# Performance work log

Measured on AMD Instinct MI355X. Metric: run time of the kernel, lower is better.

The kernel has to match this reference:

```python
import jax, jax.numpy as jnp
import numpy as np

LUT_DIM = 33
CTX_DIM = 128


def _identity_lut(dim):
    coords = jnp.linspace(0.0, 1.0, dim)
    r, g, b = jnp.meshgrid(coords, coords, coords, indexing='ij')
    return jnp.stack([r, g, b], axis=-1)  # [dim, dim, dim, 3], axes (r,g,b)


def setup_inputs() -> dict:
    key = jax.random.key(0)
    ks = jax.random.split(key, 8)
    B, H, W = 4, 512, 512
    image = jax.random.normal(ks[0], (B, 3, H, W), dtype=jnp.float32)
    spatial_context = jax.random.normal(ks[1], (B, CTX_DIM, H, W), dtype=jnp.float32)
    s = 0.05
    params = {
        'base_lut': _identity_lut(LUT_DIM),
        'W1': jax.random.normal(ks[2], (128, CTX_DIM), dtype=jnp.float32) * s,
        'b1': jnp.zeros((128,), dtype=jnp.float32),
        'W2': jax.random.normal(ks[3], (64, 128), dtype=jnp.float32) * s,
        'b2': jnp.zeros((64,), dtype=jnp.float32),
        'W3': jax.random.normal(ks[4], (3, 64), dtype=jnp.float32) * s,
        'b3': jnp.zeros((3,), dtype=jnp.float32),
        'offset_scale': jnp.float32(0.1),
    }
    return {'image': image, 'spatial_context': spatial_context, **params}


def _conv1x1(x, W, b):
    # x: [B,Cin,H,W], W: [Cout,Cin]
    return jnp.einsum('bchw,oc->bohw', x, W) + b[None, :, None, None]


def _trilinear_lut(lut_flat, gx, gy, gz, dim):
    # lut_flat: [3, dim^3] (flattened over z,y,x = r,g,b axes)
    # gx,gy,gz: [B,H,W] float coords in [0, dim-1]; border padding via clamp
    fmax = jnp.float32(dim - 1)
    gx = jnp.clip(gx, 0.0, fmax)
    gy = jnp.clip(gy, 0.0, fmax)
    gz = jnp.clip(gz, 0.0, fmax)
    x0 = jnp.floor(gx).astype(jnp.int32)
    y0 = jnp.floor(gy).astype(jnp.int32)
    z0 = jnp.floor(gz).astype(jnp.int32)
    x1 = jnp.minimum(x0 + 1, dim - 1)
    y1 = jnp.minimum(y0 + 1, dim - 1)
    z1 = jnp.minimum(z0 + 1, dim - 1)
    fx = gx - x0.astype(gx.dtype)
    fy = gy - y0.astype(gy.dtype)
    fz = gz - z0.astype(gz.dtype)

    def gather(zi, yi, xi):
        idx = (zi * dim + yi) * dim + xi  # [B,H,W]
        return lut_flat[:, idx]  # [3,B,H,W]

    c000 = gather(z0, y0, x0); c001 = gather(z0, y0, x1)
    c010 = gather(z0, y1, x0); c011 = gather(z0, y1, x1)
    c100 = gather(z1, y0, x0); c101 = gather(z1, y0, x1)
    c110 = gather(z1, y1, x0); c111 = gather(z1, y1, x1)

    fx = fx[None]; fy = fy[None]; fz = fz[None]
    c00 = c000 * (1 - fx) + c001 * fx
    c01 = c010 * (1 - fx) + c011 * fx
    c10 = c100 * (1 - fx) + c101 * fx
    c11 = c110 * (1 - fx) + c111 * fx
    c0 = c00 * (1 - fy) + c01 * fy
    c1 = c10 * (1 - fy) + c11 * fy
    out = c0 * (1 - fz) + c1 * fz  # [3,B,H,W]
    return jnp.transpose(out, (1, 0, 2, 3))  # [B,3,H,W]


def reference(image, spatial_context, base_lut, W1, b1, W2, b2, W3, b3, offset_scale):
    dim = base_lut.shape[0]
    gelu = lambda v: jax.nn.gelu(v, approximate=False)
    h = gelu(_conv1x1(spatial_context, W1, b1))
    h = gelu(_conv1x1(h, W2, b2))
    offset = jnp.tanh(_conv1x1(h, W3, b3)) * offset_scale  # [B,3,H,W]

    img01 = jnp.clip((image + 1.0) * 0.5, 0.0, 1.0)
    # grid_sample convention: grid channel0 (R)->x->last LUT axis (b),
    # channel1 (G)->y->g axis, channel2 (B)->z->r axis; align_corners=True.
    scale = jnp.float32(dim - 1)
    gx = img01[:, 0] * scale  # R -> b axis
    gy = img01[:, 1] * scale  # G -> g axis
    gz = img01[:, 2] * scale  # B -> r axis
    # base_lut [r,g,b,3] -> channels-first [3, r(=z), g(=y), b(=x)] -> flatten
    lut_flat = jnp.transpose(base_lut, (3, 0, 1, 2)).reshape(3, dim * dim * dim)
    sampled = _trilinear_lut(lut_flat, gx, gy, gz, dim)  # [B,3,H,W]
    return sampled * 2.0 - 1.0 + offset
```

## Files before the change

kernel.cpp:

```cpp
#include <hip/hip_runtime.h>
#include <stdint.h>

#define HW 262144
#define LDIM 33

typedef __bf16 bf16x8 __attribute__((ext_vector_type(8)));
typedef float  f32x4  __attribute__((ext_vector_type(4)));

union BF8 { bf16x8 v; unsigned u[4]; };

__device__ __forceinline__ unsigned bfr1(float a) {
  unsigned u = __float_as_uint(a);
  return (u + 0x7fffu + ((u >> 16) & 1u)) >> 16;
}
__device__ __forceinline__ unsigned pk2(float a, float b) {
  return bfr1(a) | (bfr1(b) << 16);
}
__device__ __forceinline__ float tanh_fast(float x) {
  return 1.0f - 2.0f / (__expf(2.0f * x) + 1.0f);
}
__device__ __forceinline__ float gelu_t(float x) {
  float t = tanh_fast(0.7978845608028654f * (x + 0.044715f * x * x * x));
  return 0.5f * x * (1.0f + t);
}

__global__ __launch_bounds__(256, 2) void local3dlut_kernel(
    const float* __restrict__ img,  const float* __restrict__ ctx,
    const float* __restrict__ lut,  const float* __restrict__ W1,
    const float* __restrict__ b1,   const float* __restrict__ W2,
    const float* __restrict__ b2,   const float* __restrict__ W3,
    const float* __restrict__ b3,   const float* __restrict__ oscp,
    float* __restrict__ out)
{
  __shared__ uint4 smem4[4096];
  char* sm = (char*)smem4;
  const int t    = threadIdx.x;
  const int lane = t & 63;
  const int wv   = t >> 6;
  const int n    = lane & 15;
  const int q    = lane >> 4;

  #pragma unroll
  for (int rep = 0; rep < 16; ++rep) {
    int f4 = t + 256 * rep;
    float4 v = ((const float4*)W1)[f4];
    int fi = f4 << 2;
    int o = fi >> 7, k = fi & 127;
    char* dst = sm + o * 256 + (((k >> 3) ^ (o & 15)) << 4) + ((k & 7) << 1);
    *(uint2*)dst = make_uint2(pk2(v.x, v.y), pk2(v.z, v.w));
  }
  #pragma unroll
  for (int rep = 0; rep < 8; ++rep) {
    int f4 = t + 256 * rep;
    float4 v = ((const float4*)W2)[f4];
    int fi = f4 << 2;
    int o = fi >> 7, k = fi & 127;
    char* dst = sm + 32768 + o * 256 + (((k >> 3) ^ (o & 15)) << 4) + ((k & 7) << 1);
    *(uint2*)dst = make_uint2(pk2(v.x, v.y), pk2(v.z, v.w));
  }
  __syncthreads();

  float b1r[8], b2r[4], w3r[3][4];
  #pragma unroll
  for (int i = 0; i < 8; ++i) b1r[i] = b1[i * 16 + n];
  #pragma unroll
  for (int i = 0; i < 4; ++i) b2r[i] = b2[i * 16 + n];
  #pragma unroll
  for (int j = 0; j < 3; ++j)
    #pragma unroll
    for (int i = 0; i < 4; ++i) w3r[j][i] = W3[j * 64 + i * 16 + n];
  const float b3r0 = b3[0], b3r1 = b3[1], b3r2 = b3[2];
  const float osc  = oscp[0];

  const int p0   = blockIdx.x * 512;
  const int bi   = p0 >> 18;
  const int sblk = p0 & (HW - 1);
  const float* ctxB = ctx + (size_t)bi * ((size_t)128 * HW);
  const float* imgB = img + (size_t)bi * ((size_t)3 * HW);
  float*       outB = out + (size_t)bi * ((size_t)3 * HW);
  char* hb = sm + 49152 + wv * 4096;

  #pragma unroll 1
  for (int it = 0; it < 4; ++it) {
    const int sw = sblk + it * 128 + wv * 32;

    BF8 a1[2][4];
    #pragma unroll
    for (int mt = 0; mt < 2; ++mt) {
      const int sA = sw + mt * 16 + n;
      #pragma unroll
      for (int ks = 0; ks < 4; ++ks) {
        const float* cb = ctxB + (size_t)(ks * 32 + q * 8) * HW + sA;
        float v0 = cb[0];
        float v1 = cb[(size_t)1 * HW];
        float v2 = cb[(size_t)2 * HW];
        float v3 = cb[(size_t)3 * HW];
        float v4 = cb[(size_t)4 * HW];
        float v5 = cb[(size_t)5 * HW];
        float v6 = cb[(size_t)6 * HW];
        float v7 = cb[(size_t)7 * HW];
        a1[mt][ks].u[0] = pk2(v0, v1);
        a1[mt][ks].u[1] = pk2(v2, v3);
        a1[mt][ks].u[2] = pk2(v4, v5);
        a1[mt][ks].u[3] = pk2(v6, v7);
      }
    }

    f32x4 acc2[2][4];
    #pragma unroll
    for (int mt = 0; mt < 2; ++mt)
      #pragma unroll
      for (int j = 0; j < 4; ++j) { f32x4 z = {0.f,0.f,0.f,0.f}; acc2[mt][j] = z; }

    #pragma unroll
    for (int half = 0; half < 2; ++half) {
      f32x4 acc1[2][4];
      #pragma unroll
      for (int mt = 0; mt < 2; ++mt)
        #pragma unroll
        for (int j = 0; j < 4; ++j) { f32x4 z = {0.f,0.f,0.f,0.f}; acc1[mt][j] = z; }

      #pragma unroll
      for (int ks = 0; ks < 4; ++ks) {
        #pragma unroll
        for (int nt4 = 0; nt4 < 4; ++nt4) {
          int row = (half * 4 + nt4) * 16 + n;
          bf16x8 bw = *(const bf16x8*)(sm + row * 256 + ((((ks << 2) + q) ^ n) << 4));
          acc1[0][nt4] = __builtin_amdgcn_mfma_f32_16x16x32_bf16(a1[0][ks].v, bw, acc1[0][nt4], 0, 0, 0);
          acc1[1][nt4] = __builtin_amdgcn_mfma_f32_16x16x32_bf16(a1[1][ks].v, bw, acc1[1][nt4], 0, 0, 0);
        }
      }
      #pragma unroll
      for (int mt = 0; mt < 2; ++mt)
        #pragma unroll
        for (int nt4 = 0; nt4 < 4; ++nt4) {
          int fl = nt4 * 16 + n;
          int kgf = fl >> 3;
          #pragma unroll
          for (int r = 0; r < 4; ++r) {
            int px = mt * 16 + (q << 2) + r;
            float hv = gelu_t(acc1[mt][nt4][r] + b1r[half * 4 + nt4]);
            *(unsigned short*)(hb + px * 128 + ((kgf ^ (px & 7)) << 4) + ((fl & 7) << 1)) =
                (unsigned short)bfr1(hv);
          }
        }
      #pragma unroll
      for (int ks2 = 0; ks2 < 2; ++ks2) {
        bf16x8 a2[2];
        #pragma unroll
        for (int mt = 0; mt < 2; ++mt) {
          int px = mt * 16 + n;
          a2[mt] = *(const bf16x8*)(hb + px * 128 + ((((ks2 << 2) + q) ^ (px & 7)) << 4));
        }
        #pragma unroll
        for (int nt2 = 0; nt2 < 4; ++nt2) {
          int row = nt2 * 16 + n;
          int kg2 = half * 8 + (ks2 << 2) + q;
          bf16x8 bw = *(const bf16x8*)(sm + 32768 + row * 256 + ((kg2 ^ n) << 4));
          acc2[0][nt2] = __builtin_amdgcn_mfma_f32_16x16x32_bf16(a2[0], bw, acc2[0][nt2], 0, 0, 0);
          acc2[1][nt2] = __builtin_amdgcn_mfma_f32_16x16x32_bf16(a2[1], bw, acc2[1][nt2], 0, 0, 0);
        }
      }
    }

    #pragma unroll
    for (int mt = 0; mt < 2; ++mt)
      #pragma unroll
      for (int nt2 = 0; nt2 < 4; ++nt2)
        #pragma unroll
        for (int r = 0; r < 4; ++r)
          acc2[mt][nt2][r] = gelu_t(acc2[mt][nt2][r] + b2r[nt2]);

    #pragma unroll
    for (int mt = 0; mt < 2; ++mt)
      #pragma unroll
      for (int r = 0; r < 4; ++r) {
        float h0 = acc2[mt][0][r], h1v = acc2[mt][1][r], h2v = acc2[mt][2][r], h3v = acc2[mt][3][r];
        float pa = w3r[0][0]*h0 + w3r[0][1]*h1v + w3r[0][2]*h2v + w3r[0][3]*h3v;
        float pb = w3r[1][0]*h0 + w3r[1][1]*h1v + w3r[1][2]*h2v + w3r[1][3]*h3v;
        float pc = w3r[2][0]*h0 + w3r[2][1]*h1v + w3r[2][2]*h2v + w3r[2][3]*h3v;
        pa += __shfl_xor(pa, 1, 16); pa += __shfl_xor(pa, 2, 16);
        pa += __shfl_xor(pa, 4, 16); pa += __shfl_xor(pa, 8, 16);
        pb += __shfl_xor(pb, 1, 16); pb += __shfl_xor(pb, 2, 16);
        pb += __shfl_xor(pb, 4, 16); pb += __shfl_xor(pb, 8, 16);
        pc += __shfl_xor(pc, 1, 16); pc += __shfl_xor(pc, 2, 16);
        pc += __shfl_xor(pc, 4, 16); pc += __shfl_xor(pc, 8, 16);
        int px = mt * 16 + (q << 2) + r;
        float sel  = (n == 0) ? pa   : ((n == 1) ? pb   : pc);
        float bsel = (n == 0) ? b3r0 : ((n == 1) ? b3r1 : b3r2);
        float ov = tanh_fast(sel + bsel) * osc;
        if (n < 3) *(float*)(hb + px * 12 + (n << 2)) = ov;
      }

    if (lane < 32) {
      const int sp = sw + lane;
      float o0 = *(const float*)(hb + lane * 12 + 0);
      float o1 = *(const float*)(hb + lane * 12 + 4);
      float o2 = *(const float*)(hb + lane * 12 + 8);

      float rr = imgB[sp], gg = imgB[HW + sp], bb = imgB[2 * HW + sp];
      float gx = fminf(fmaxf((rr + 1.f) * 0.5f, 0.f), 1.f) * 32.f;
      float gy = fminf(fmaxf((gg + 1.f) * 0.5f, 0.f), 1.f) * 32.f;
      float gz = fminf(fmaxf((bb + 1.f) * 0.5f, 0.f), 1.f) * 32.f;
      int x0 = (int)gx, y0 = (int)gy, z0 = (int)gz;
      float fx = gx - (float)x0, fy = gy - (float)y0, fz = gz - (float)z0;
      int x1 = min(x0 + 1, 32), y1 = min(y0 + 1, 32), z1 = min(z0 + 1, 32);
      int zy00 = (z0 * LDIM + y0) * LDIM, zy01 = (z0 * LDIM + y1) * LDIM;
      int zy10 = (z1 * LDIM + y0) * LDIM, zy11 = (z1 * LDIM + y1) * LDIM;
      int i000 = (zy00 + x0) * 3, i001 = (zy00 + x1) * 3;
      int i010 = (zy01 + x0) * 3, i011 = (zy01 + x1) * 3;
      int i100 = (zy10 + x0) * 3, i101 = (zy10 + x1) * 3;
      int i110 = (zy11 + x0) * 3, i111 = (zy11 + x1) * 3;
      const float* L = lut;
      float so[3];
      #pragma unroll
      for (int ch = 0; ch < 3; ++ch) {
        float c000 = L[i000 + ch], c001 = L[i001 + ch];
        float c010 = L[i010 + ch], c011 = L[i011 + ch];
        float c100 = L[i100 + ch], c101 = L[i101 + ch];
        float c110 = L[i110 + ch], c111 = L[i111 + ch];
        float c00 = c000 + fx * (c001 - c000);
        float c01 = c010 + fx * (c011 - c010);
        float c10 = c100 + fx * (c101 - c100);
        float c11 = c110 + fx * (c111 - c110);
        float ca  = c00 + fy * (c01 - c00);
        float cb2 = c10 + fy * (c11 - c10);
        so[ch] = ca + fz * (cb2 - ca);
      }
      outB[sp]          = so[0] * 2.f - 1.f + o0;
      outB[HW + sp]     = so[1] * 2.f - 1.f + o1;
      outB[2 * HW + sp] = so[2] * 2.f - 1.f + o2;
    }
  }
}

extern "C" void kernel_launch(void* const* d_in, const int* in_sizes, int n_in,
                              void* d_out, int out_size, void* d_ws, size_t ws_size,
                              hipStream_t stream) {
  const float* img = (const float*)d_in[0];
  const float* ctx = (const float*)d_in[1];
  const float* lut = (const float*)d_in[2];
  const float* W1  = (const float*)d_in[3];
  const float* b1  = (const float*)d_in[4];
  const float* W2  = (const float*)d_in[5];
  const float* b2  = (const float*)d_in[6];
  const float* W3  = (const float*)d_in[7];
  const float* b3  = (const float*)d_in[8];
  const float* osc = (const float*)d_in[9];
  float* out = (float*)d_out;
  local3dlut_kernel<<<dim3(2048), dim3(256), 0, stream>>>(
      img, ctx, lut, W1, b1, W2, b2, W3, b3, osc, out);
}
```

Before: 831.7 us.

## Transpose MFMA chain to keep activations in registers and prefetch context

The MLP chain now puts weights on the A operand and pixels on the B operand. Each layer's GELU output can then be packed straight into the next MFMA's B fragment, with no round trip through an LDS staging buffer. Layer 3 becomes an MFMA using W3 stored in LDS, in place of the shuffle reductions. Context loads for the next iteration are issued early into registers (software prefetch) so they overlap compute. Biases move to LDS, occupancy is raised to 3 blocks per SM, and the bf16 pack uses the library conversion. The prefetch buffers raise register pressure, which may conflict with the higher occupancy target.

```diff
diff --git a/kernel.cpp b/kernel.cpp
--- a/kernel.cpp
+++ b/kernel.cpp
@@ -1,4 +1,5 @@
 #include <hip/hip_runtime.h>
+#include <hip/hip_bf16.h>
 #include <stdint.h>
 
 #define HW 262144
@@ -9,12 +10,16 @@
 
 union BF8 { bf16x8 v; unsigned u[4]; };
 
-__device__ __forceinline__ unsigned bfr1(float a) {
-  unsigned u = __float_as_uint(a);
-  return (u + 0x7fffu + ((u >> 16) & 1u)) >> 16;
-}
+#define W1OFS 0
+#define W2OFS 32768
+#define W3OFS 49152
+#define B1OFS 51200
+#define B2OFS 51712
+#define SMBYTES 51968
+
 __device__ __forceinline__ unsigned pk2(float a, float b) {
-  return bfr1(a) | (bfr1(b) << 16);
+  __hip_bfloat162 h = __float22bfloat162_rn(make_float2(a, b));
+  union { __hip_bfloat162 h; unsigned u; } c; c.h = h; return c.u;
 }
 __device__ __forceinline__ float tanh_fast(float x) {
   return 1.0f - 2.0f / (__expf(2.0f * x) + 1.0f);
@@ -24,7 +29,16 @@
   return 0.5f * x * (1.0f + t);
 }
 
-__global__ __launch_bounds__(256, 2) void local3dlut_kernel(
+__device__ __forceinline__ void issue_ctx(const float* __restrict__ cb0, float vr[4][8]) {
+  #pragma unroll
+  for (int ks = 0; ks < 4; ++ks)
+    #pragma unroll
+    for (int j = 0; j < 8; ++j)
+      vr[ks][j] = cb0[(size_t)(ks * 32 + j) * HW];
+}
+
+
+__global__ __launch_bounds__(256, 3) void local3dlut_kernel(
     const float* __restrict__ img,  const float* __restrict__ ctx,
     const float* __restrict__ lut,  const float* __restrict__ W1,
     const float* __restrict__ b1,   const float* __restrict__ W2,
@@ -32,7 +46,7 @@
     const float* __restrict__ b3,   const float* __restrict__ oscp,
     float* __restrict__ out)
 {
-  __shared__ uint4 smem4[4096];
+  __shared__ uint4 smem4[SMBYTES / 16];
   char* sm = (char*)smem4;
   const int t    = threadIdx.x;
   const int lane = t & 63;
@@ -46,31 +60,32 @@
     float4 v = ((const float4*)W1)[f4];
     int fi = f4 << 2;
     int o = fi >> 7, k = fi & 127;
-    char* dst = sm + o * 256 + (((k >> 3) ^ (o & 15)) << 4) + ((k & 7) << 1);
+    char* dst = sm + W1OFS + o * 256 + (((k >> 3) ^ (o & 15)) << 4) + ((k & 7) << 1);
     *(uint2*)dst = make_uint2(pk2(v.x, v.y), pk2(v.z, v.w));
   }
   #pragma unroll
   for (int rep = 0; rep < 8; ++rep) {
-    int f4 = t + 256 * rep;
-    float4 v = ((const float4*)W2)[f4];
-    int fi = f4 << 2;
-    int o = fi >> 7, k = fi & 127;
-    char* dst = sm + 32768 + o * 256 + (((k >> 3) ^ (o & 15)) << 4) + ((k & 7) << 1);
+    int idx = t + 256 * rep;
+    int f2 = idx >> 5, rem = idx & 31, g2 = rem >> 1, jh = rem & 1;
+    int f1b = 32 * (g2 >> 2) + 16 * jh + 4 * (g2 & 3);
+    float4 v = *(const float4*)(W2 + f2 * 128 + f1b);
+    char* dst = sm + W2OFS + f2 * 256 + ((g2 ^ (f2 & 15)) << 4) + jh * 8;
     *(uint2*)dst = make_uint2(pk2(v.x, v.y), pk2(v.z, v.w));
   }
+  {
+    int c = t >> 4, rem = t & 15, g3 = rem >> 1, jh = rem & 1;
+    int f2b = 32 * (g3 >> 2) + 16 * jh + 4 * (g3 & 3);
+    float4 v = make_float4(0.f, 0.f, 0.f, 0.f);
+    if (c < 3) v = *(const float4*)(W3 + c * 64 + f2b);
+    char* dst = sm + W3OFS + c * 128 + ((g3 ^ (c & 7)) << 4) + jh * 8;
+    *(uint2*)dst = make_uint2(pk2(v.x, v.y), pk2(v.z, v.w));
+  }
+  if (t < 128) ((float*)(sm + B1OFS))[t] = b1[t];
+  if (t < 64)  ((float*)(sm + B2OFS))[t] = b2[t];
   __syncthreads();
 
-  float b1r[8], b2r[4], w3r[3][4];
-  #pragma unroll
-  for (int i = 0; i < 8; ++i) b1r[i] = b1[i * 16 + n];
-  #pragma unroll
-  for (int i = 0; i < 4; ++i) b2r[i] = b2[i * 16 + n];
-  #pragma unroll
-  for (int j = 0; j < 3; ++j)
-    #pragma unroll
-    for (int i = 0; i < 4; ++i) w3r[j][i] = W3[j * 64 + i * 16 + n];
-  const float b3r0 = b3[0], b3r1 = b3[1], b3r2 = b3[2];
-  const float osc  = oscp[0];
+  const float b3r[3] = { b3[0], b3[1], b3[2] };
+  const float osc = oscp[0];
 
   const int p0   = blockIdx.x * 512;
   const int bi   = p0 >> 18;
@@ -78,125 +93,136 @@
   const float* ctxB = ctx + (size_t)bi * ((size_t)128 * HW);
   const float* imgB = img + (size_t)bi * ((size_t)3 * HW);
   float*       outB = out + (size_t)bi * ((size_t)3 * HW);
-  char* hb = sm + 49152 + wv * 4096;
+
+  const size_t laneChOfs = (size_t)(q * 8) * HW;
+
+  float vr0[4][8], vr1[4][8];
+  {
+    const int sw = sblk + wv * 32;
+    issue_ctx(ctxB + laneChOfs + (sw + 0  + n), vr0);
+    issue_ctx(ctxB + laneChOfs + (sw + 16 + n), vr1);
+  }
 
   #pragma unroll 1
   for (int it = 0; it < 4; ++it) {
     const int sw = sblk + it * 128 + wv * 32;
 
-    BF8 a1[2][4];
-    #pragma unroll
-    for (int mt = 0; mt < 2; ++mt) {
-      const int sA = sw + mt * 16 + n;
+    BF8 fr[2][4];
+    #pragma unroll
+    for (int ks = 0; ks < 4; ++ks) {
+      #pragma unroll
+      for (int i = 0; i < 4; ++i) {
+        fr[0][ks].u[i] = pk2(vr0[ks][2 * i], vr0[ks][2 * i + 1]);
+        fr[1][ks].u[i] = pk2(vr1[ks][2 * i], vr1[ks][2 * i + 1]);
+      }
+    }
+    if (it < 3) {
+      const int swn = sblk + (it + 1) * 128 + wv * 32;
+      issue_ctx(ctxB + laneChOfs + (swn + n), vr0);
+    }
+
+    f32x4 acc2[4][2];
+    #pragma unroll
+    for (int n2 = 0; n2 < 4; ++n2)
+      #pragma unroll
+      for (int mt = 0; mt < 2; ++mt) { f32x4 z = {0.f,0.f,0.f,0.f}; acc2[n2][mt] = z; }
+
+    #pragma unroll
+    for (int h = 0; h < 2; ++h) {
+      f32x4 acc1[4][2];
+      #pragma unroll
+      for (int nf = 0; nf < 4; ++nf)
+        #pragma unroll
+        for (int mt = 0; mt < 2; ++mt) { f32x4 z = {0.f,0.f,0.f,0.f}; acc1[nf][mt] = z; }
+
       #pragma unroll
       for (int ks = 0; ks < 4; ++ks) {
-        const float* cb = ctxB + (size_t)(ks * 32 + q * 8) * HW + sA;
-        float v0 = cb[0];
-        float v1 = cb[(size_t)1 * HW];
-        float v2 = cb[(size_t)2 * HW];
-        float v3 = cb[(size_t)3 * HW];
-        float v4 = cb[(size_t)4 * HW];
-        float v5 = cb[(size_t)5 * HW];
-        float v6 = cb[(size_t)6 * HW];
-        float v7 = cb[(size_t)7 * HW];
-        a1[mt][ks].u[0] = pk2(v0, v1);
-        a1[mt][ks].u[1] = pk2(v2, v3);
-        a1[mt][ks].u[2] = pk2(v4, v5);
-        a1[mt][ks].u[3] = pk2(v6, v7);
-      }
-    }
-
-    f32x4 acc2[2][4];
-    #pragma unroll
-    for (int mt = 0; mt < 2; ++mt)
-      #pragma unroll
-      for (int j = 0; j < 4; ++j) { f32x4 z = {0.f,0.f,0.f,0.f}; acc2[mt][j] = z; }
-
-    #pragma unroll
-    for (int half = 0; half < 2; ++half) {
-      f32x4 acc1[2][4];
-      #pragma unroll
-      for (int mt = 0; mt < 2; ++mt)
-        #pragma unroll
-        for (int j = 0; j < 4; ++j) { f32x4 z = {0.f,0.f,0.f,0.f}; acc1[mt][j] = z; }
-
-      #pragma unroll
-      for (int ks = 0; ks < 4; ++ks) {
-        #pragma unroll
-        for (int nt4 = 0; nt4 < 4; ++nt4) {
-          int row = (half * 4 + nt4) * 16 + n;
-          bf16x8 bw = *(const bf16x8*)(sm + row * 256 + ((((ks << 2) + q) ^ n) << 4));
-          acc1[0][nt4] = __builtin_amdgcn_mfma_f32_16x16x32_bf16(a1[0][ks].v, bw, acc1[0][nt4], 0, 0, 0);
-          acc1[1][nt4] = __builtin_amdgcn_mfma_f32_16x16x32_bf16(a1[1][ks].v, bw, acc1[1][nt4], 0, 0, 0);
-        }
-      }
-      #pragma unroll
-      for (int mt = 0; mt < 2; ++mt)
-        #pragma unroll
-        for (int nt4 = 0; nt4 < 4; ++nt4) {
-          int fl = nt4 * 16 + n;
-          int kgf = fl >> 3;
-          #pragma unroll
-          for (int r = 0; r < 4; ++r) {
-            int px = mt * 16 + (q << 2) + r;
-            float hv = gelu_t(acc1[mt][nt4][r] + b1r[half * 4 + nt4]);
-            *(unsigned short*)(hb + px * 128 + ((kgf ^ (px & 7)) << 4) + ((fl & 7) << 1)) =
-                (unsigned short)bfr1(hv);
-          }
-        }
-      #pragma unroll
-      for (int ks2 = 0; ks2 < 2; ++ks2) {
-        bf16x8 a2[2];
+        #pragma unroll
+        for (int nf = 0; nf < 4; ++nf) {
+          int row = (h * 4 + nf) * 16 + n;
+          bf16x8 aw = *(const bf16x8*)(sm + W1OFS + row * 256 + ((((ks << 2) + q) ^ n) << 4));
+          acc1[nf][0] = __builtin_amdgcn_mfma_f32_16x16x32_bf16(aw, fr[0][ks].v, acc1[nf][0], 0, 0, 0);
+          acc1[nf][1] = __builtin_amdgcn_mfma_f32_16x16x32_bf16(aw, fr[1][ks].v, acc1[nf][1], 0, 0, 0);
+        }
+      }
+      unsigned pd[4][2][2];
+      #pragma unroll
+      for (int nf = 0; nf < 4; ++nf) {
+        f32x4 bb = *(const f32x4*)(sm + B1OFS + (h * 64 + nf * 16 + 4 * q) * 4);
         #pragma unroll
         for (int mt = 0; mt < 2; ++mt) {
-          int px = mt * 16 + n;
-          a2[mt] = *(const bf16x8*)(hb + px * 128 + ((((ks2 << 2) + q) ^ (px & 7)) << 4));
-        }
-        #pragma unroll
-        for (int nt2 = 0; nt2 < 4; ++nt2) {
-          int row = nt2 * 16 + n;
-          int kg2 = half * 8 + (ks2 << 2) + q;
-          bf16x8 bw = *(const bf16x8*)(sm + 32768 + row * 256 + ((kg2 ^ n) << 4));
-          acc2[0][nt2] = __builtin_amdgcn_mfma_f32_16x16x32_bf16(a2[0], bw, acc2[0][nt2], 0, 0, 0);
-          acc2[1][nt2] = __builtin_amdgcn_mfma_f32_16x16x32_bf16(a2[1], bw, acc2[1][nt2], 0, 0, 0);
-        }
-      }
-    }
-
-    #pragma unroll
-    for (int mt = 0; mt < 2; ++mt)
-      #pragma unroll
-      for (int nt2 = 0; nt2 < 4; ++nt2)
-        #pragma unroll
-        for (int r = 0; r < 4; ++r)
-          acc2[mt][nt2][r] = gelu_t(acc2[mt][nt2][r] + b2r[nt2]);
-
-    #pragma unroll
-    for (int mt = 0; mt < 2; ++mt)
-      #pragma unroll
-      for (int r = 0; r < 4; ++r) {
-        float h0 = acc2[mt][0][r], h1v = acc2[mt][1][r], h2v = acc2[mt][2][r], h3v = acc2[mt][3][r];
-        float pa = w3r[0][0]*h0 + w3r[0][1]*h1v + w3r[0][2]*h2v + w3r[0][3]*h3v;
-        float pb = w3r[1][0]*h0 + w3r[1][1]*h1v + w3r[1][2]*h2v + w3r[1][3]*h3v;
-        float pc = w3r[2][0]*h0 + w3r[2][1]*h1v + w3r[2][2]*h2v + w3r[2][3]*h3v;
-        pa += __shfl_xor(pa, 1, 16); pa += __shfl_xor(pa, 2, 16);
-        pa += __shfl_xor(pa, 4, 16); pa += __shfl_xor(pa, 8, 16);
-        pb += __shfl_xor(pb, 1, 16); pb += __shfl_xor(pb, 2, 16);
-        pb += __shfl_xor(pb, 4, 16); pb += __shfl_xor(pb, 8, 16);
-        pc += __shfl_xor(pc, 1, 16); pc += __shfl_xor(pc, 2, 16);
-        pc += __shfl_xor(pc, 4, 16); pc += __shfl_xor(pc, 8, 16);
-        int px = mt * 16 + (q << 2) + r;
-        float sel  = (n == 0) ? pa   : ((n == 1) ? pb   : pc);
-        float bsel = (n == 0) ? b3r0 : ((n == 1) ? b3r1 : b3r2);
-        float ov = tanh_fast(sel + bsel) * osc;
-        if (n < 3) *(float*)(hb + px * 12 + (n << 2)) = ov;
-      }
-
+          float g0 = gelu_t(acc1[nf][mt][0] + bb[0]);
+          float g1 = gelu_t(acc1[nf][mt][1] + bb[1]);
+          float g2 = gelu_t(acc1[nf][mt][2] + bb[2]);
+          float g3 = gelu_t(acc1[nf][mt][3] + bb[3]);
+          pd[nf][mt][0] = pk2(g0, g1);
+          pd[nf][mt][1] = pk2(g2, g3);
+        }
+      }
+      #pragma unroll
+      for (int k2 = 0; k2 < 2; ++k2) {
+        int ks2g = 2 * h + k2;
+        BF8 bfr[2];
+        #pragma unroll
+        for (int mt = 0; mt < 2; ++mt) {
+          bfr[mt].u[0] = pd[2 * k2][mt][0];     bfr[mt].u[1] = pd[2 * k2][mt][1];
+          bfr[mt].u[2] = pd[2 * k2 + 1][mt][0]; bfr[mt].u[3] = pd[2 * k2 + 1][mt][1];
+        }
+        #pragma unroll
+        for (int n2 = 0; n2 < 4; ++n2) {
+          int row = n2 * 16 + n;
+          bf16x8 aw = *(const bf16x8*)(sm + W2OFS + row * 256 + ((((ks2g << 2) + q) ^ n) << 4));
+          acc2[n2][0] = __builtin_amdgcn_mfma_f32_16x16x32_bf16(aw, bfr[0].v, acc2[n2][0], 0, 0, 0);
+          acc2[n2][1] = __builtin_amdgcn_mfma_f32_16x16x32_bf16(aw, bfr[1].v, acc2[n2][1], 0, 0, 0);
+        }
+      }
+    }
+
+    if (it < 3) {
+      const int swn = sblk + (it + 1) * 128 + wv * 32;
+      issue_ctx(ctxB + laneChOfs + (swn + 16 + n), vr1);
+    }
+
+    unsigned pd2[4][2][2];
+    #pragma unroll
+    for (int n2 = 0; n2 < 4; ++n2) {
+      f32x4 bb = *(const f32x4*)(sm + B2OFS + (n2 * 16 + 4 * q) * 4);
+      #pragma unroll
+      for (int mt = 0; mt < 2; ++mt) {
+        float g0 = gelu_t(acc2[n2][mt][0] + bb[0]);
+        float g1 = gelu_t(acc2[n2][mt][1] + bb[1]);
+        float g2 = gelu_t(acc2[n2][mt][2] + bb[2]);
+        float g3 = gelu_t(acc2[n2][mt][3] + bb[3]);
+        pd2[n2][mt][0] = pk2(g0, g1);
+        pd2[n2][mt][1] = pk2(g2, g3);
+      }
+    }
+    f32x4 acc3[2];
+    { f32x4 z = {0.f,0.f,0.f,0.f}; acc3[0] = z; acc3[1] = z; }
+    #pragma unroll
+    for (int k3 = 0; k3 < 2; ++k3) {
+      bf16x8 aw = *(const bf16x8*)(sm + W3OFS + n * 128 + ((((k3 << 2) + q) ^ (n & 7)) << 4));
+      #pragma unroll
+      for (int mt = 0; mt < 2; ++mt) {
+        BF8 bfr;
+        bfr.u[0] = pd2[2 * k3][mt][0];     bfr.u[1] = pd2[2 * k3][mt][1];
+        bfr.u[2] = pd2[2 * k3 + 1][mt][0]; bfr.u[3] = pd2[2 * k3 + 1][mt][1];
+        acc3[mt] = __builtin_amdgcn_mfma_f32_16x16x32_bf16(aw, bfr.v, acc3[mt], 0, 0, 0);
+      }
+    }
+
+    float oc[3];
+    #pragma unroll
+    for (int c = 0; c < 3; ++c) {
+      float a0 = __shfl(acc3[0][c], n, 64);
+      float a1 = __shfl(acc3[1][c], n, 64);
+      oc[c] = (lane & 16) ? a1 : a0;
+    }
     if (lane < 32) {
       const int sp = sw + lane;
-      float o0 = *(const float*)(hb + lane * 12 + 0);
-      float o1 = *(const float*)(hb + lane * 12 + 4);
-      float o2 = *(const float*)(hb + lane * 12 + 8);
+      float ov[3];
+      #pragma unroll
+      for (int c = 0; c < 3; ++c) ov[c] = tanh_fast(oc[c] + b3r[c]) * osc;
 
       float rr = imgB[sp], gg = imgB[HW + sp], bb = imgB[2 * HW + sp];
       float gx = fminf(fmaxf((rr + 1.f) * 0.5f, 0.f), 1.f) * 32.f;
@@ -227,9 +253,9 @@
         float cb2 = c10 + fy * (c11 - c10);
         so[ch] = ca + fz * (cb2 - ca);
       }
-      outB[sp]          = so[0] * 2.f - 1.f + o0;
-      outB[HW + sp]     = so[1] * 2.f - 1.f + o1;
-      outB[2 * HW + sp] = so[2] * 2.f - 1.f + o2;
+      outB[sp]          = so[0] * 2.f - 1.f + ov[0];
+      outB[HW + sp]     = so[1] * 2.f - 1.f + ov[1];
+      outB[2 * HW + sp] = so[2] * 2.f - 1.f + ov[2];
     }
   }
 }
```

New measurement: 1.490 ms. 1.79x slower.
